# Performance work log

Hardware: AMD Instinct MI355X
Metric: run time of the kernel (lower is better)

The kernel has to match this reference:

```python
import jax, jax.numpy as jnp
import numpy as np

BOND = 64    # bond_dim
FEAT = 32    # feature_dim (after dropping flag channel)
B = 256      # batch
T = 512      # input_len
OUT = 32     # output_dim


def setup_inputs() -> dict:
    key = jax.random.key(0)
    k1, k2, k3, k4 = jax.random.split(key, 4)
    # channel 0 is the 'presence flag' (=1), remaining FEAT channels are small features,
    # so each transfer matrix is ~ I + small perturbation (stable 512-long chain product).
    x_feat = 0.05 * jax.random.normal(k1, (B, T, FEAT), dtype=jnp.float32)
    x = jnp.concatenate([jnp.ones((B, T, 1), dtype=jnp.float32), x_feat], axis=-1)  # (B,T,FEAT+1)
    # batch_core: slice 0 is identity (flag channel), slices 1: are the learned core
    tensor_core = jnp.zeros((BOND, FEAT + 1, BOND), dtype=jnp.float32)
    tensor_core = tensor_core.at[:, 0, :].set(jnp.eye(BOND, dtype=jnp.float32))
    tensor_core = tensor_core.at[:, 1:, :].set(
        0.02 * jax.random.normal(k2, (BOND, FEAT, BOND), dtype=jnp.float32))
    alpha = jax.random.normal(k3, (BOND,), dtype=jnp.float32)          # left boundary vector
    output_core = (jnp.eye(BOND, OUT, dtype=jnp.float32)
                   + 0.01 * jax.random.normal(k4, (BOND, OUT), dtype=jnp.float32))
    return {"x": x, "tensor_core": tensor_core, "alpha": alpha, "output_core": output_core}


def reference(x, tensor_core, alpha, output_core):
    # UMPS with input_nn_depth=0 (identity input NN, no softmax) and output node at the end:
    #   out[b] = alpha^T * prod_t M_t[b] * output_core,  M_t[b] = sum_f x[b,t,f] * core[:,f,:]
    # Contract left-to-right with a (B, bond) vector carry (never materializes M for all t).
    xs = jnp.swapaxes(x, 0, 1)  # (T, B, F+1)
    v0 = jnp.broadcast_to(alpha[None, :], (x.shape[0], alpha.shape[0]))  # (B, bond)

    def step(v, x_t):
        # A[b] = sum_f x_t[b,f] * core[:,f,:]  -> (B, bond, bond)
        A = jnp.einsum('bf,ifj->bij', x_t, tensor_core)
        return jnp.einsum('bi,bij->bj', v, A), None

    vT, _ = jax.lax.scan(step, v0, xs)  # (B, bond)
    return vT @ output_core             # (B, OUT)
```

## Files before the change

kernel.cpp:

```cpp
#include <hip/hip_runtime.h>

#define NB    256
#define NT    512
#define NF    33
#define BOND  64
#define NOUT  32
#define TC    64
#define NCH   (NT / TC)
#define MSTR  4104

typedef _Float16 f16x4 __attribute__((ext_vector_type(4)));
typedef _Float16 f16x8 __attribute__((ext_vector_type(8)));
typedef float    f32x4 __attribute__((ext_vector_type(4)));

__global__ __launch_bounds__(64) void pack_cfrag(const float* __restrict__ core,
                                                 _Float16* __restrict__ cfrag)
{
    int tid = blockIdx.x * 64 + threadIdx.x;
    int nt = tid >> 6, l = tid & 63;
    int g = l >> 4, c = l & 15;
    int n = nt * 16 + c;
    int i = n & 63, j = n >> 6;
    const float* src = core + (size_t)i * (NF * BOND) + (size_t)(1 + g * 8) * BOND + j;
    f16x8 v;
    #pragma unroll
    for (int m = 0; m < 8; ++m) v[m] = (_Float16)src[(size_t)m * BOND];
    *(f16x8*)(cfrag + (size_t)tid * 8) = v;
}

__global__ __launch_bounds__(512, 1) void chunk_prod(const float* __restrict__ x,
                                                     const _Float16* __restrict__ cfrag,
                                                     float* __restrict__ Pout)
{
    __shared__ __align__(16) _Float16 PB[2][64 * 64];
    __shared__ __align__(16) _Float16 Mb[16 * MSTR];
    __shared__ __align__(16) _Float16 Xl[TC][32];
    __shared__ float x0l[TC];

    const int tid = (int)threadIdx.x;
    const int l = tid & 63, w = tid >> 6;
    const int g = l >> 4, c = l & 15;
    const int ch = (int)blockIdx.x, b = (int)blockIdx.y;

    const float* xb = x + (size_t)b * (NT * NF) + (size_t)(ch * TC) * NF;
    for (int idx = tid; idx < TC * NF; idx += 512) {
        int t = idx / NF, f = idx - t * NF;
        float v = xb[idx];
        if (f == 0) x0l[t] = v;
        else        Xl[t][f - 1] = (_Float16)v;
    }
    for (int idx = tid; idx < 4096; idx += 512) {
        int row = idx >> 6, col = idx & 63;
        PB[0][row * 64 + (col ^ ((row & 7) << 3))] = (row == col) ? (_Float16)1.f : (_Float16)0.f;
    }

    f16x8 creg[32];
    {
        const _Float16* cf = cfrag + (size_t)w * 16384 + (size_t)l * 8;
        #pragma unroll
        for (int q = 0; q < 32; ++q) creg[q] = *(const f16x8*)(cf + (size_t)q * 512);
    }
    __syncthreads();

    const int sw = (c & 7) << 3;
    const int rb = (w >> 1) << 4;
    const int cb = (w & 1) << 5;
    const int arow = rb + c;
    const int wcol = (cb + 4 * g) ^ sw;

    int pcur = 0;
    #pragma unroll 1
    for (int fr = 0; fr < 4; ++fr) {
        f16x8 xa  = *(const f16x8*)&Xl[fr * 16 + c][g * 8];
        float x0v = x0l[fr * 16 + c];
        #pragma unroll
        for (int q = 0; q < 32; ++q) {
            int nt = w * 32 + q;
            f32x4 zero = {0.f, 0.f, 0.f, 0.f};
            f32x4 d = __builtin_amdgcn_mfma_f32_16x16x32_f16(creg[q], xa, zero, 0, 0, 0);
            int j  = nt >> 2;
            int i0 = ((nt & 3) << 4) + (g << 2);
            int dr = j - i0;
            f16x4 mv;
            mv[0] = (_Float16)((dr == 0) ? d[0] + x0v : d[0]);
            mv[1] = (_Float16)((dr == 1) ? d[1] + x0v : d[1]);
            mv[2] = (_Float16)((dr == 2) ? d[2] + x0v : d[2]);
            mv[3] = (_Float16)((dr == 3) ? d[3] + x0v : d[3]);
            *(f16x4*)(&Mb[c * MSTR + (j << 6) + (i0 ^ ((j & 7) << 3))]) = mv;
        }
        __syncthreads();

        #pragma unroll 4
        for (int s = 0; s < 16; ++s) {
            const _Float16* Ms = &Mb[s * MSTR];
            const _Float16* Ps = &PB[pcur][0];
            f16x8 a0  = *(const f16x8*)&Ps[arow * 64 + ((g * 8)      ^ sw)];
            f16x8 a1  = *(const f16x8*)&Ps[arow * 64 + ((32 + g * 8) ^ sw)];
            f16x8 b00 = *(const f16x8*)&Ms[(cb + c) * 64      + ((g * 8)      ^ sw)];
            f16x8 b01 = *(const f16x8*)&Ms[(cb + c) * 64      + ((32 + g * 8) ^ sw)];
            f16x8 b10 = *(const f16x8*)&Ms[(cb + 16 + c) * 64 + ((g * 8)      ^ sw)];
            f16x8 b11 = *(const f16x8*)&Ms[(cb + 16 + c) * 64 + ((32 + g * 8) ^ sw)];
            f32x4 acc0 = {0.f, 0.f, 0.f, 0.f}, acc1 = {0.f, 0.f, 0.f, 0.f};
            acc0 = __builtin_amdgcn_mfma_f32_16x16x32_f16(b00, a0, acc0, 0, 0, 0);
            acc0 = __builtin_amdgcn_mfma_f32_16x16x32_f16(b01, a1, acc0, 0, 0, 0);
            acc1 = __builtin_amdgcn_mfma_f32_16x16x32_f16(b10, a0, acc1, 0, 0, 0);
            acc1 = __builtin_amdgcn_mfma_f32_16x16x32_f16(b11, a1, acc1, 0, 0, 0);

            if (fr == 3 && s == 15) {
                float* Po = Pout + (size_t)(b * NCH + ch) * 4096;
                *(f32x4*)(Po + arow * 64 + cb + 4 * g)      = acc0;
                *(f32x4*)(Po + arow * 64 + cb + 16 + 4 * g) = acc1;
            } else {
                _Float16* Pn = &PB[pcur ^ 1][0];
                f16x4 v0, v1;
                v0[0] = (_Float16)acc0[0]; v0[1] = (_Float16)acc0[1];
                v0[2] = (_Float16)acc0[2]; v0[3] = (_Float16)acc0[3];
                v1[0] = (_Float16)acc1[0]; v1[1] = (_Float16)acc1[1];
                v1[2] = (_Float16)acc1[2]; v1[3] = (_Float16)acc1[3];
                *(f16x4*)(Pn + arow * 64 + wcol)        = v0;
                *(f16x4*)(Pn + arow * 64 + (wcol ^ 16)) = v1;
            }
            __syncthreads();
            pcur ^= 1;
        }
    }
}

__global__ __launch_bounds__(256) void combine(const float* __restrict__ P,
                                               const float* __restrict__ alpha,
                                               const float* __restrict__ oc,
                                               float* __restrict__ out)
{
    const int b = (int)blockIdx.x;
    const int tid = (int)threadIdx.x, j = tid & 63, q = tid >> 6;
    __shared__ float vb[BOND];
    __shared__ float ps[4][BOND];
    if (tid < BOND) vb[tid] = alpha[tid];
    __syncthreads();
    for (int ch = 0; ch < NCH; ++ch) {
        const float* Pc = P + (size_t)(b * NCH + ch) * 4096;
        float s = 0.f;
        #pragma unroll
        for (int k = 0; k < 16; ++k) {
            int i = q * 16 + k;
            s = fmaf(vb[i], Pc[i * 64 + j], s);
        }
        ps[q][j] = s;
        __syncthreads();
        if (q == 0) vb[j] = (ps[0][j] + ps[1][j]) + (ps[2][j] + ps[3][j]);
        __syncthreads();
    }
    if (tid < NOUT) {
        float s = 0.f;
        #pragma unroll 8
        for (int i = 0; i < BOND; ++i) s = fmaf(vb[i], oc[i * NOUT + tid], s);
        out[b * NOUT + tid] = s;
    }
}

extern "C" void kernel_launch(void* const* d_in, const int* in_sizes, int n_in,
                              void* d_out, int out_size, void* d_ws, size_t ws_size,
                              hipStream_t stream)
{
    const float* x     = (const float*)d_in[0];
    const float* core  = (const float*)d_in[1];
    const float* alpha = (const float*)d_in[2];
    const float* oc    = (const float*)d_in[3];
    float* out = (float*)d_out;

    _Float16* cfrag = (_Float16*)d_ws;
    float*    P     = (float*)((char*)d_ws + 262144);

    pack_cfrag<<<dim3(256), dim3(64), 0, stream>>>(core, cfrag);
    chunk_prod<<<dim3(NCH, NB), dim3(512), 0, stream>>>(x, cfrag, P);
    combine<<<dim3(NB), dim3(256), 0, stream>>>(P, alpha, oc, out);
}
```

Measured before the change: 244.7 us.

## Replace sequential per-step chain products with tree reduction over 16 slices

```diff
diff --git a/kernel.cpp b/kernel.cpp
--- a/kernel.cpp
+++ b/kernel.cpp
@@ -7,11 +7,13 @@
 #define NOUT  32
 #define TC    64
 #define NCH   (NT / TC)
-#define MSTR  4104
+#define SLC   4096
 
 typedef _Float16 f16x4 __attribute__((ext_vector_type(4)));
 typedef _Float16 f16x8 __attribute__((ext_vector_type(8)));
 typedef float    f32x4 __attribute__((ext_vector_type(4)));
+
+#define MFMA16(a, b, c) __builtin_amdgcn_mfma_f32_16x16x32_f16((a), (b), (c), 0, 0, 0)
 
 __global__ __launch_bounds__(64) void pack_cfrag(const float* __restrict__ core,
                                                  _Float16* __restrict__ cfrag)
@@ -28,12 +30,89 @@
     *(f16x8*)(cfrag + (size_t)tid * 8) = v;
 }
 
+__device__ __forceinline__ f16x8 ldf(const _Float16* base, int row16, int c, int kh,
+                                     int g, int sw)
+{
+    return *(const f16x8*)(base + (row16 * 16 + c) * 64 + ((((kh) << 5) + (g << 3)) ^ sw));
+}
+
+template<int NRB, int NCB, bool F32OUT>
+__device__ __forceinline__ void prod_tiles(const _Float16* __restrict__ U,
+                                           const _Float16* __restrict__ V,
+                                           _Float16* O, float* FO,
+                                           int rb0, int cb0, int g, int c, int sw)
+{
+    f16x8 uf[NCB][2], vf[NRB][2];
+    #pragma unroll
+    for (int cb = 0; cb < NCB; ++cb) {
+        uf[cb][0] = ldf(U, cb0 + cb, c, 0, g, sw);
+        uf[cb][1] = ldf(U, cb0 + cb, c, 1, g, sw);
+    }
+    #pragma unroll
+    for (int rb = 0; rb < NRB; ++rb) {
+        vf[rb][0] = ldf(V, rb0 + rb, c, 0, g, sw);
+        vf[rb][1] = ldf(V, rb0 + rb, c, 1, g, sw);
+    }
+    #pragma unroll
+    for (int rb = 0; rb < NRB; ++rb) {
+        const int row = (rb0 + rb) * 16 + c;
+        #pragma unroll
+        for (int cb = 0; cb < NCB; ++cb) {
+            f32x4 acc = {0.f, 0.f, 0.f, 0.f};
+            acc = MFMA16(uf[cb][0], vf[rb][0], acc);
+            acc = MFMA16(uf[cb][1], vf[rb][1], acc);
+            const int col0 = (cb0 + cb) * 16 + (g << 2);
+            if (F32OUT) {
+                *(f32x4*)(FO + row * 64 + col0) = acc;
+            } else {
+                f16x4 hv;
+                hv[0] = (_Float16)acc[0]; hv[1] = (_Float16)acc[1];
+                hv[2] = (_Float16)acc[2]; hv[3] = (_Float16)acc[3];
+                *(f16x4*)(O + row * 64 + (col0 ^ sw)) = hv;
+            }
+        }
+    }
+}
+
+__device__ __forceinline__ void transpose_slice(_Float16* Sl, int g, int c, int sw)
+{
+    f16x8 uf[4][2];
+    #pragma unroll
+    for (int cb = 0; cb < 4; ++cb) {
+        uf[cb][0] = ldf(Sl, cb, c, 0, g, sw);
+        uf[cb][1] = ldf(Sl, cb, c, 1, g, sw);
+    }
+    #pragma unroll
+    for (int rb = 0; rb < 4; ++rb) {
+        const int row = rb * 16 + c;
+        f16x8 iv[2];
+        #pragma unroll
+        for (int kh = 0; kh < 2; ++kh) {
+            const int p = rb * 16 + c - (kh * 32 + g * 8);
+            #pragma unroll
+            for (int m = 0; m < 8; ++m)
+                iv[kh][m] = (_Float16)((p == m) ? 1.f : 0.f);
+        }
+        #pragma unroll
+        for (int cb = 0; cb < 4; ++cb) {
+            f32x4 acc = {0.f, 0.f, 0.f, 0.f};
+            acc = MFMA16(uf[cb][0], iv[0], acc);
+            acc = MFMA16(uf[cb][1], iv[1], acc);
+            const int col0 = cb * 16 + (g << 2);
+            f16x4 hv;
+            hv[0] = (_Float16)acc[0]; hv[1] = (_Float16)acc[1];
+            hv[2] = (_Float16)acc[2]; hv[3] = (_Float16)acc[3];
+            *(f16x4*)(Sl + row * 64 + (col0 ^ sw)) = hv;
+        }
+    }
+}
+
 __global__ __launch_bounds__(512, 1) void chunk_prod(const float* __restrict__ x,
                                                      const _Float16* __restrict__ cfrag,
                                                      float* __restrict__ Pout)
 {
+    __shared__ __align__(16) _Float16 Mb[16 * SLC];
     __shared__ __align__(16) _Float16 PB[2][64 * 64];
-    __shared__ __align__(16) _Float16 Mb[16 * MSTR];
     __shared__ __align__(16) _Float16 Xl[TC][32];
     __shared__ float x0l[TC];
 
@@ -41,6 +120,7 @@
     const int l = tid & 63, w = tid >> 6;
     const int g = l >> 4, c = l & 15;
     const int ch = (int)blockIdx.x, b = (int)blockIdx.y;
+    const int sw = (c & 7) << 3;
 
     const float* xb = x + (size_t)b * (NT * NF) + (size_t)(ch * TC) * NF;
     for (int idx = tid; idx < TC * NF; idx += 512) {
@@ -62,13 +142,9 @@
     }
     __syncthreads();
 
-    const int sw = (c & 7) << 3;
-    const int rb = (w >> 1) << 4;
-    const int cb = (w & 1) << 5;
-    const int arow = rb + c;
-    const int wcol = (cb + 4 * g) ^ sw;
-
     int pcur = 0;
+    float* Po = Pout + (size_t)(b * NCH + ch) * 4096;
+
     #pragma unroll 1
     for (int fr = 0; fr < 4; ++fr) {
         f16x8 xa  = *(const f16x8*)&Xl[fr * 16 + c][g * 8];
@@ -77,7 +153,7 @@
         for (int q = 0; q < 32; ++q) {
             int nt = w * 32 + q;
             f32x4 zero = {0.f, 0.f, 0.f, 0.f};
-            f32x4 d = __builtin_amdgcn_mfma_f32_16x16x32_f16(creg[q], xa, zero, 0, 0, 0);
+            f32x4 d = MFMA16(creg[q], xa, zero);
             int j  = nt >> 2;
             int i0 = ((nt & 3) << 4) + (g << 2);
             int dr = j - i0;
@@ -86,43 +162,50 @@
             mv[1] = (_Float16)((dr == 1) ? d[1] + x0v : d[1]);
             mv[2] = (_Float16)((dr == 2) ? d[2] + x0v : d[2]);
             mv[3] = (_Float16)((dr == 3) ? d[3] + x0v : d[3]);
-            *(f16x4*)(&Mb[c * MSTR + (j << 6) + (i0 ^ ((j & 7) << 3))]) = mv;
-        }
-        __syncthreads();
-
-        #pragma unroll 4
-        for (int s = 0; s < 16; ++s) {
-            const _Float16* Ms = &Mb[s * MSTR];
-            const _Float16* Ps = &PB[pcur][0];
-            f16x8 a0  = *(const f16x8*)&Ps[arow * 64 + ((g * 8)      ^ sw)];
-            f16x8 a1  = *(const f16x8*)&Ps[arow * 64 + ((32 + g * 8) ^ sw)];
-            f16x8 b00 = *(const f16x8*)&Ms[(cb + c) * 64      + ((g * 8)      ^ sw)];
-            f16x8 b01 = *(const f16x8*)&Ms[(cb + c) * 64      + ((32 + g * 8) ^ sw)];
-            f16x8 b10 = *(const f16x8*)&Ms[(cb + 16 + c) * 64 + ((g * 8)      ^ sw)];
-            f16x8 b11 = *(const f16x8*)&Ms[(cb + 16 + c) * 64 + ((32 + g * 8) ^ sw)];
-            f32x4 acc0 = {0.f, 0.f, 0.f, 0.f}, acc1 = {0.f, 0.f, 0.f, 0.f};
-            acc0 = __builtin_amdgcn_mfma_f32_16x16x32_f16(b00, a0, acc0, 0, 0, 0);
-            acc0 = __builtin_amdgcn_mfma_f32_16x16x32_f16(b01, a1, acc0, 0, 0, 0);
-            acc1 = __builtin_amdgcn_mfma_f32_16x16x32_f16(b10, a0, acc1, 0, 0, 0);
-            acc1 = __builtin_amdgcn_mfma_f32_16x16x32_f16(b11, a1, acc1, 0, 0, 0);
-
-            if (fr == 3 && s == 15) {
-                float* Po = Pout + (size_t)(b * NCH + ch) * 4096;
-                *(f32x4*)(Po + arow * 64 + cb + 4 * g)      = acc0;
-                *(f32x4*)(Po + arow * 64 + cb + 16 + 4 * g) = acc1;
-            } else {
-                _Float16* Pn = &PB[pcur ^ 1][0];
-                f16x4 v0, v1;
-                v0[0] = (_Float16)acc0[0]; v0[1] = (_Float16)acc0[1];
-                v0[2] = (_Float16)acc0[2]; v0[3] = (_Float16)acc0[3];
-                v1[0] = (_Float16)acc1[0]; v1[1] = (_Float16)acc1[1];
-                v1[2] = (_Float16)acc1[2]; v1[3] = (_Float16)acc1[3];
-                *(f16x4*)(Pn + arow * 64 + wcol)        = v0;
-                *(f16x4*)(Pn + arow * 64 + (wcol ^ 16)) = v1;
-            }
-            __syncthreads();
+            *(f16x4*)(&Mb[c * SLC + (j << 6) + (i0 ^ ((j & 7) << 3))]) = mv;
+        }
+        __syncthreads();
+
+        _Float16* Se = &Mb[(2 * w) * SLC];
+        _Float16* So = &Mb[(2 * w + 1) * SLC];
+        transpose_slice(Se, g, c, sw);
+        if (w & 1) prod_tiles<4, 4, false>(Se, So, Se, nullptr, 0, 0, g, c, sw);
+        else       prod_tiles<4, 4, false>(So, Se, Se, nullptr, 0, 0, g, c, sw);
+        __syncthreads();
+
+        {
+            int k = w >> 1, h = w & 1;
+            const _Float16* A = &Mb[(4 * k) * SLC];
+            const _Float16* B = &Mb[(4 * k + 2) * SLC];
+            _Float16* O = &Mb[(4 * k + 1) * SLC];
+            if (k & 1) prod_tiles<2, 4, false>(A, B, O, nullptr, 2 * h, 0, g, c, sw);
+            else       prod_tiles<2, 4, false>(B, A, O, nullptr, 2 * h, 0, g, c, sw);
+        }
+        __syncthreads();
+
+        {
+            int p = w >> 2, h = w & 3;
+            const _Float16* A = &Mb[(8 * p + 1) * SLC];
+            const _Float16* B = &Mb[(8 * p + 5) * SLC];
+            _Float16* O = &Mb[(8 * p + 3) * SLC];
+            if (p & 1) prod_tiles<1, 4, false>(A, B, O, nullptr, h, 0, g, c, sw);
+            else       prod_tiles<1, 4, false>(B, A, O, nullptr, h, 0, g, c, sw);
+        }
+        __syncthreads();
+
+        prod_tiles<1, 2, false>(&Mb[3 * SLC], &Mb[11 * SLC], &Mb[7 * SLC], nullptr,
+                                w >> 1, 2 * (w & 1), g, c, sw);
+        __syncthreads();
+
+        if (fr == 3) {
+            prod_tiles<1, 2, true>(&Mb[7 * SLC], &PB[pcur][0], nullptr, Po,
+                                   w >> 1, 2 * (w & 1), g, c, sw);
+        } else {
+            prod_tiles<1, 2, false>(&Mb[7 * SLC], &PB[pcur][0], &PB[pcur ^ 1][0], nullptr,
+                                    w >> 1, 2 * (w & 1), g, c, sw);
             pcur ^= 1;
         }
+        __syncthreads();
     }
 }
 
```

Result: slower. 439.1 us (+79.4%).

## Warp-specialize chunk product into producer and consumer waves with row-strip chains

Applied to the files above, without the earlier changes.

```diff
diff --git a/kernel.cpp b/kernel.cpp
--- a/kernel.cpp
+++ b/kernel.cpp
@@ -7,11 +7,12 @@
 #define NOUT  32
 #define TC    64
 #define NCH   (NT / TC)
-#define MSTR  4104
 
 typedef _Float16 f16x4 __attribute__((ext_vector_type(4)));
 typedef _Float16 f16x8 __attribute__((ext_vector_type(8)));
 typedef float    f32x4 __attribute__((ext_vector_type(4)));
+
+#define MFMA16(a, b, c) __builtin_amdgcn_mfma_f32_16x16x32_f16((a), (b), (c), 0, 0, 0)
 
 __global__ __launch_bounds__(64) void pack_cfrag(const float* __restrict__ core,
                                                  _Float16* __restrict__ cfrag)
@@ -28,101 +29,114 @@
     *(f16x8*)(cfrag + (size_t)tid * 8) = v;
 }
 
-__global__ __launch_bounds__(512, 1) void chunk_prod(const float* __restrict__ x,
+__global__ __launch_bounds__(512, 2) void chunk_prod(const float* __restrict__ x,
                                                      const _Float16* __restrict__ cfrag,
                                                      float* __restrict__ Pout)
 {
-    __shared__ __align__(16) _Float16 PB[2][64 * 64];
-    __shared__ __align__(16) _Float16 Mb[16 * MSTR];
-    __shared__ __align__(16) _Float16 Xl[TC][32];
+    __shared__ __align__(16) _Float16 Mb[2][8 * 4096];
+    __shared__ __align__(16) _Float16 Pst[4][16 * 64];
+    __shared__ __align__(16) _Float16 Xl[TC * 32];
     __shared__ float x0l[TC];
 
     const int tid = (int)threadIdx.x;
     const int l = tid & 63, w = tid >> 6;
     const int g = l >> 4, c = l & 15;
     const int ch = (int)blockIdx.x, b = (int)blockIdx.y;
+    const int sw = (c & 7) << 3;
 
     const float* xb = x + (size_t)b * (NT * NF) + (size_t)(ch * TC) * NF;
     for (int idx = tid; idx < TC * NF; idx += 512) {
         int t = idx / NF, f = idx - t * NF;
         float v = xb[idx];
         if (f == 0) x0l[t] = v;
-        else        Xl[t][f - 1] = (_Float16)v;
-    }
-    for (int idx = tid; idx < 4096; idx += 512) {
-        int row = idx >> 6, col = idx & 63;
-        PB[0][row * 64 + (col ^ ((row & 7) << 3))] = (row == col) ? (_Float16)1.f : (_Float16)0.f;
-    }
-
-    f16x8 creg[32];
-    {
-        const _Float16* cf = cfrag + (size_t)w * 16384 + (size_t)l * 8;
-        #pragma unroll
-        for (int q = 0; q < 32; ++q) creg[q] = *(const f16x8*)(cf + (size_t)q * 512);
+        else        Xl[t * 32 + (f - 1)] = (_Float16)v;
     }
     __syncthreads();
 
-    const int sw = (c & 7) << 3;
-    const int rb = (w >> 1) << 4;
-    const int cb = (w & 1) << 5;
-    const int arow = rb + c;
-    const int wcol = (cb + 4 * g) ^ sw;
+    if (w >= 4) {
+        const int fw = w - 4;
+        const int sl = c & 7, sx = sl << 3;
+        const _Float16* cf0 = cfrag + ((size_t)(fw * 64) * 64 + (size_t)l) * 8;
+        f16x8 creg[32];
+        #pragma unroll
+        for (int q = 0; q < 32; ++q) creg[q] = *(const f16x8*)(cf0 + (size_t)q * 512);
 
-    int pcur = 0;
-    #pragma unroll 1
-    for (int fr = 0; fr < 4; ++fr) {
-        f16x8 xa  = *(const f16x8*)&Xl[fr * 16 + c][g * 8];
-        float x0v = x0l[fr * 16 + c];
-        #pragma unroll
-        for (int q = 0; q < 32; ++q) {
-            int nt = w * 32 + q;
-            f32x4 zero = {0.f, 0.f, 0.f, 0.f};
-            f32x4 d = __builtin_amdgcn_mfma_f32_16x16x32_f16(creg[q], xa, zero, 0, 0, 0);
-            int j  = nt >> 2;
-            int i0 = ((nt & 3) << 4) + (g << 2);
-            int dr = j - i0;
-            f16x4 mv;
-            mv[0] = (_Float16)((dr == 0) ? d[0] + x0v : d[0]);
-            mv[1] = (_Float16)((dr == 1) ? d[1] + x0v : d[1]);
-            mv[2] = (_Float16)((dr == 2) ? d[2] + x0v : d[2]);
-            mv[3] = (_Float16)((dr == 3) ? d[3] + x0v : d[3]);
-            *(f16x4*)(&Mb[c * MSTR + (j << 6) + (i0 ^ ((j & 7) << 3))]) = mv;
-        }
-        __syncthreads();
-
-        #pragma unroll 4
-        for (int s = 0; s < 16; ++s) {
-            const _Float16* Ms = &Mb[s * MSTR];
-            const _Float16* Ps = &PB[pcur][0];
-            f16x8 a0  = *(const f16x8*)&Ps[arow * 64 + ((g * 8)      ^ sw)];
-            f16x8 a1  = *(const f16x8*)&Ps[arow * 64 + ((32 + g * 8) ^ sw)];
-            f16x8 b00 = *(const f16x8*)&Ms[(cb + c) * 64      + ((g * 8)      ^ sw)];
-            f16x8 b01 = *(const f16x8*)&Ms[(cb + c) * 64      + ((32 + g * 8) ^ sw)];
-            f16x8 b10 = *(const f16x8*)&Ms[(cb + 16 + c) * 64 + ((g * 8)      ^ sw)];
-            f16x8 b11 = *(const f16x8*)&Ms[(cb + 16 + c) * 64 + ((32 + g * 8) ^ sw)];
-            f32x4 acc0 = {0.f, 0.f, 0.f, 0.f}, acc1 = {0.f, 0.f, 0.f, 0.f};
-            acc0 = __builtin_amdgcn_mfma_f32_16x16x32_f16(b00, a0, acc0, 0, 0, 0);
-            acc0 = __builtin_amdgcn_mfma_f32_16x16x32_f16(b01, a1, acc0, 0, 0, 0);
-            acc1 = __builtin_amdgcn_mfma_f32_16x16x32_f16(b10, a0, acc1, 0, 0, 0);
-            acc1 = __builtin_amdgcn_mfma_f32_16x16x32_f16(b11, a1, acc1, 0, 0, 0);
-
-            if (fr == 3 && s == 15) {
-                float* Po = Pout + (size_t)(b * NCH + ch) * 4096;
-                *(f32x4*)(Po + arow * 64 + cb + 4 * g)      = acc0;
-                *(f32x4*)(Po + arow * 64 + cb + 16 + 4 * g) = acc1;
-            } else {
-                _Float16* Pn = &PB[pcur ^ 1][0];
-                f16x4 v0, v1;
-                v0[0] = (_Float16)acc0[0]; v0[1] = (_Float16)acc0[1];
-                v0[2] = (_Float16)acc0[2]; v0[3] = (_Float16)acc0[3];
-                v1[0] = (_Float16)acc1[0]; v1[1] = (_Float16)acc1[1];
-                v1[2] = (_Float16)acc1[2]; v1[3] = (_Float16)acc1[3];
-                *(f16x4*)(Pn + arow * 64 + wcol)        = v0;
-                *(f16x4*)(Pn + arow * 64 + (wcol ^ 16)) = v1;
+        #pragma unroll 1
+        for (int gi = 0; gi < 8; ++gi) {
+            _Float16* Mg = Mb[gi & 1];
+            f16x8 xa = *(const f16x8*)(Xl + (gi * 8 + sl) * 32 + 8 * g);
+            float x0v = x0l[gi * 8 + sl];
+            #pragma unroll
+            for (int q = 0; q < 64; ++q) {
+                int nt = fw * 64 + q;
+                f16x8 ca = (q < 32) ? creg[q] : *(const f16x8*)(cf0 + (size_t)q * 512);
+                f32x4 z = {0.f, 0.f, 0.f, 0.f};
+                f32x4 d = MFMA16(ca, xa, z);
+                int j  = nt >> 2;
+                int i0 = ((nt & 3) << 4) + (g << 2);
+                int dr = j - i0;
+                f16x4 mv;
+                mv[0] = (_Float16)((dr == 0) ? d[0] + x0v : d[0]);
+                mv[1] = (_Float16)((dr == 1) ? d[1] + x0v : d[1]);
+                mv[2] = (_Float16)((dr == 2) ? d[2] + x0v : d[2]);
+                mv[3] = (_Float16)((dr == 3) ? d[3] + x0v : d[3]);
+                *(f16x4*)(&Mg[sl * 4096 + (j << 6) + (i0 ^ ((j & 7) << 3) ^ sx)]) = mv;
             }
             __syncthreads();
-            pcur ^= 1;
         }
+    } else {
+        _Float16* Pw = &Pst[w][0];
+        f16x8 a0, a1;
+        #pragma unroll
+        for (int m = 0; m < 8; ++m) {
+            a0[m] = (_Float16)(((16 * w + c) == (8 * g + m)) ? 1.f : 0.f);
+            a1[m] = (_Float16)(((16 * w + c) == (32 + 8 * g + m)) ? 1.f : 0.f);
+        }
+        f32x4 q0, q1, q2, q3;
+        #pragma unroll 1
+        for (int r = 0; r < 8; ++r) {
+            __syncthreads();
+            const _Float16* Mg = Mb[r & 1];
+            #pragma unroll
+            for (int s = 0; s < 8; ++s) {
+                const _Float16* Ms = Mg + s * 4096;
+                const int kx0 = (8 * g) ^ sw ^ (s << 3);
+                const int kx1 = kx0 ^ 32;
+                f16x8 b00 = *(const f16x8*)(Ms + (c)      * 64 + kx0);
+                f16x8 b01 = *(const f16x8*)(Ms + (c)      * 64 + kx1);
+                f16x8 b10 = *(const f16x8*)(Ms + (16 + c) * 64 + kx0);
+                f16x8 b11 = *(const f16x8*)(Ms + (16 + c) * 64 + kx1);
+                f16x8 b20 = *(const f16x8*)(Ms + (32 + c) * 64 + kx0);
+                f16x8 b21 = *(const f16x8*)(Ms + (32 + c) * 64 + kx1);
+                f16x8 b30 = *(const f16x8*)(Ms + (48 + c) * 64 + kx0);
+                f16x8 b31 = *(const f16x8*)(Ms + (48 + c) * 64 + kx1);
+                f32x4 z = {0.f, 0.f, 0.f, 0.f};
+                q0 = MFMA16(b00, a0, z); q0 = MFMA16(b01, a1, q0);
+                q1 = MFMA16(b10, a0, z); q1 = MFMA16(b11, a1, q1);
+                q2 = MFMA16(b20, a0, z); q2 = MFMA16(b21, a1, q2);
+                q3 = MFMA16(b30, a0, z); q3 = MFMA16(b31, a1, q3);
+                if (!(r == 7 && s == 7)) {
+                    f16x4 h0, h1, h2, h3;
+                    h0[0]=(_Float16)q0[0]; h0[1]=(_Float16)q0[1]; h0[2]=(_Float16)q0[2]; h0[3]=(_Float16)q0[3];
+                    h1[0]=(_Float16)q1[0]; h1[1]=(_Float16)q1[1]; h1[2]=(_Float16)q1[2]; h1[3]=(_Float16)q1[3];
+                    h2[0]=(_Float16)q2[0]; h2[1]=(_Float16)q2[1]; h2[2]=(_Float16)q2[2]; h2[3]=(_Float16)q2[3];
+                    h3[0]=(_Float16)q3[0]; h3[1]=(_Float16)q3[1]; h3[2]=(_Float16)q3[2]; h3[3]=(_Float16)q3[3];
+                    const int wc = (4 * g) ^ sw;
+                    *(f16x4*)(Pw + c * 64 + wc)        = h0;
+                    *(f16x4*)(Pw + c * 64 + (wc ^ 16)) = h1;
+                    *(f16x4*)(Pw + c * 64 + (wc ^ 32)) = h2;
+                    *(f16x4*)(Pw + c * 64 + (wc ^ 48)) = h3;
+                    a0 = *(const f16x8*)(Pw + c * 64 + ((8 * g) ^ sw));
+                    a1 = *(const f16x8*)(Pw + c * 64 + ((32 + 8 * g) ^ sw));
+                }
+            }
+        }
+        float* Po = Pout + (size_t)(b * NCH + ch) * 4096;
+        const int prow = 16 * w + c;
+        *(f32x4*)(Po + prow * 64 +  0 + 4 * g) = q0;
+        *(f32x4*)(Po + prow * 64 + 16 + 4 * g) = q1;
+        *(f32x4*)(Po + prow * 64 + 32 + 4 * g) = q2;
+        *(f32x4*)(Po + prow * 64 + 48 + 4 * g) = q3;
     }
 }
 
```

Result: slower. 436.7 us (+78.5%).

## Stream core fragments from global, shrink M buffer to 8 steps, single-buffer P

Applied to the files above, without the earlier changes.

```diff
diff --git a/kernel.cpp b/kernel.cpp
--- a/kernel.cpp
+++ b/kernel.cpp
@@ -7,11 +7,12 @@
 #define NOUT  32
 #define TC    64
 #define NCH   (NT / TC)
-#define MSTR  4104
 
 typedef _Float16 f16x4 __attribute__((ext_vector_type(4)));
 typedef _Float16 f16x8 __attribute__((ext_vector_type(8)));
 typedef float    f32x4 __attribute__((ext_vector_type(4)));
+
+#define MFMA16(a, b, c) __builtin_amdgcn_mfma_f32_16x16x32_f16((a), (b), (c), 0, 0, 0)
 
 __global__ __launch_bounds__(64) void pack_cfrag(const float* __restrict__ core,
                                                  _Float16* __restrict__ cfrag)
@@ -32,52 +33,46 @@
                                                      const _Float16* __restrict__ cfrag,
                                                      float* __restrict__ Pout)
 {
-    __shared__ __align__(16) _Float16 PB[2][64 * 64];
-    __shared__ __align__(16) _Float16 Mb[16 * MSTR];
-    __shared__ __align__(16) _Float16 Xl[TC][32];
+    __shared__ __align__(16) _Float16 Mb[8 * 4096];
+    __shared__ __align__(16) _Float16 PB[64 * 64];
+    __shared__ __align__(16) _Float16 Xl[TC * 32];
     __shared__ float x0l[TC];
 
     const int tid = (int)threadIdx.x;
     const int l = tid & 63, w = tid >> 6;
     const int g = l >> 4, c = l & 15;
     const int ch = (int)blockIdx.x, b = (int)blockIdx.y;
+    const int sw = (c & 7) << 3;
 
     const float* xb = x + (size_t)b * (NT * NF) + (size_t)(ch * TC) * NF;
     for (int idx = tid; idx < TC * NF; idx += 512) {
         int t = idx / NF, f = idx - t * NF;
         float v = xb[idx];
         if (f == 0) x0l[t] = v;
-        else        Xl[t][f - 1] = (_Float16)v;
+        else        Xl[t * 32 + (f - 1)] = (_Float16)v;
     }
     for (int idx = tid; idx < 4096; idx += 512) {
         int row = idx >> 6, col = idx & 63;
-        PB[0][row * 64 + (col ^ ((row & 7) << 3))] = (row == col) ? (_Float16)1.f : (_Float16)0.f;
-    }
-
-    f16x8 creg[32];
-    {
-        const _Float16* cf = cfrag + (size_t)w * 16384 + (size_t)l * 8;
-        #pragma unroll
-        for (int q = 0; q < 32; ++q) creg[q] = *(const f16x8*)(cf + (size_t)q * 512);
+        PB[row * 64 + (col ^ ((row & 7) << 3))] = (row == col) ? (_Float16)1.f : (_Float16)0.f;
     }
     __syncthreads();
 
-    const int sw = (c & 7) << 3;
     const int rb = (w >> 1) << 4;
     const int cb = (w & 1) << 5;
     const int arow = rb + c;
-    const int wcol = (cb + 4 * g) ^ sw;
+    const int sl = c & 7, sx = sl << 3;
+    const _Float16* cf0 = cfrag + ((size_t)(w * 32) * 64 + (size_t)l) * 8;
 
-    int pcur = 0;
     #pragma unroll 1
-    for (int fr = 0; fr < 4; ++fr) {
-        f16x8 xa  = *(const f16x8*)&Xl[fr * 16 + c][g * 8];
-        float x0v = x0l[fr * 16 + c];
-        #pragma unroll
+    for (int gi = 0; gi < 8; ++gi) {
+        f16x8 xa  = *(const f16x8*)(Xl + (gi * 8 + sl) * 32 + 8 * g);
+        float x0v = x0l[gi * 8 + sl];
+        #pragma unroll 4
         for (int q = 0; q < 32; ++q) {
             int nt = w * 32 + q;
-            f32x4 zero = {0.f, 0.f, 0.f, 0.f};
-            f32x4 d = __builtin_amdgcn_mfma_f32_16x16x32_f16(creg[q], xa, zero, 0, 0, 0);
+            f16x8 ca = *(const f16x8*)(cf0 + (size_t)q * 512);
+            f32x4 z = {0.f, 0.f, 0.f, 0.f};
+            f32x4 d = MFMA16(ca, xa, z);
             int j  = nt >> 2;
             int i0 = ((nt & 3) << 4) + (g << 2);
             int dr = j - i0;
@@ -86,42 +81,43 @@
             mv[1] = (_Float16)((dr == 1) ? d[1] + x0v : d[1]);
             mv[2] = (_Float16)((dr == 2) ? d[2] + x0v : d[2]);
             mv[3] = (_Float16)((dr == 3) ? d[3] + x0v : d[3]);
-            *(f16x4*)(&Mb[c * MSTR + (j << 6) + (i0 ^ ((j & 7) << 3))]) = mv;
+            *(f16x4*)(&Mb[sl * 4096 + (j << 6) + (i0 ^ ((j & 7) << 3) ^ sx)]) = mv;
         }
         __syncthreads();
 
-        #pragma unroll 4
-        for (int s = 0; s < 16; ++s) {
-            const _Float16* Ms = &Mb[s * MSTR];
-            const _Float16* Ps = &PB[pcur][0];
-            f16x8 a0  = *(const f16x8*)&Ps[arow * 64 + ((g * 8)      ^ sw)];
-            f16x8 a1  = *(const f16x8*)&Ps[arow * 64 + ((32 + g * 8) ^ sw)];
-            f16x8 b00 = *(const f16x8*)&Ms[(cb + c) * 64      + ((g * 8)      ^ sw)];
-            f16x8 b01 = *(const f16x8*)&Ms[(cb + c) * 64      + ((32 + g * 8) ^ sw)];
-            f16x8 b10 = *(const f16x8*)&Ms[(cb + 16 + c) * 64 + ((g * 8)      ^ sw)];
-            f16x8 b11 = *(const f16x8*)&Ms[(cb + 16 + c) * 64 + ((32 + g * 8) ^ sw)];
+        #pragma unroll
+        for (int s = 0; s < 8; ++s) {
+            const _Float16* Ms = Mb + s * 4096;
+            const int kx0 = (8 * g) ^ sw ^ (s << 3);
+            const int kx1 = kx0 ^ 32;
+            f16x8 a0  = *(const f16x8*)(PB + arow * 64 + ((8 * g) ^ sw));
+            f16x8 a1  = *(const f16x8*)(PB + arow * 64 + ((32 + 8 * g) ^ sw));
+            f16x8 b00 = *(const f16x8*)(Ms + (cb + c) * 64      + kx0);
+            f16x8 b01 = *(const f16x8*)(Ms + (cb + c) * 64      + kx1);
+            f16x8 b10 = *(const f16x8*)(Ms + (cb + 16 + c) * 64 + kx0);
+            f16x8 b11 = *(const f16x8*)(Ms + (cb + 16 + c) * 64 + kx1);
+            __syncthreads();
             f32x4 acc0 = {0.f, 0.f, 0.f, 0.f}, acc1 = {0.f, 0.f, 0.f, 0.f};
-            acc0 = __builtin_amdgcn_mfma_f32_16x16x32_f16(b00, a0, acc0, 0, 0, 0);
-            acc0 = __builtin_amdgcn_mfma_f32_16x16x32_f16(b01, a1, acc0, 0, 0, 0);
-            acc1 = __builtin_amdgcn_mfma_f32_16x16x32_f16(b10, a0, acc1, 0, 0, 0);
-            acc1 = __builtin_amdgcn_mfma_f32_16x16x32_f16(b11, a1, acc1, 0, 0, 0);
+            acc0 = MFMA16(b00, a0, acc0);
+            acc0 = MFMA16(b01, a1, acc0);
+            acc1 = MFMA16(b10, a0, acc1);
+            acc1 = MFMA16(b11, a1, acc1);
 
-            if (fr == 3 && s == 15) {
+            if (gi == 7 && s == 7) {
                 float* Po = Pout + (size_t)(b * NCH + ch) * 4096;
                 *(f32x4*)(Po + arow * 64 + cb + 4 * g)      = acc0;
                 *(f32x4*)(Po + arow * 64 + cb + 16 + 4 * g) = acc1;
             } else {
-                _Float16* Pn = &PB[pcur ^ 1][0];
-                f16x4 v0, v1;
-                v0[0] = (_Float16)acc0[0]; v0[1] = (_Float16)acc0[1];
-                v0[2] = (_Float16)acc0[2]; v0[3] = (_Float16)acc0[3];
-                v1[0] = (_Float16)acc1[0]; v1[1] = (_Float16)acc1[1];
-                v1[2] = (_Float16)acc1[2]; v1[3] = (_Float16)acc1[3];
-                *(f16x4*)(Pn + arow * 64 + wcol)        = v0;
-                *(f16x4*)(Pn + arow * 64 + (wcol ^ 16)) = v1;
+                f16x4 h0, h1;
+                h0[0] = (_Float16)acc0[0]; h0[1] = (_Float16)acc0[1];
+                h0[2] = (_Float16)acc0[2]; h0[3] = (_Float16)acc0[3];
+                h1[0] = (_Float16)acc1[0]; h1[1] = (_Float16)acc1[1];
+                h1[2] = (_Float16)acc1[2]; h1[3] = (_Float16)acc1[3];
+                const int wcol = (cb + 4 * g) ^ sw;
+                *(f16x4*)(PB + arow * 64 + wcol)        = h0;
+                *(f16x4*)(PB + arow * 64 + (wcol ^ 16)) = h1;
+                if (s != 7) __syncthreads();
             }
-            __syncthreads();
-            pcur ^= 1;
         }
     }
 }
```

After: 350.0 us. 1.43x slower.
